# Kernel tuning notes

Hardware: AMD Instinct MI355X
Metric: run time of the kernel (lower is better)

The kernel has to match this reference:

```python
import jax, jax.numpy as jnp
import numpy as np

EPS = 1e-5
GROUPS = 32


def _groupnorm(x, gamma, beta):
    B, C, H, W = x.shape
    xr = x.reshape(B, GROUPS, C // GROUPS, H, W)
    mu = xr.mean(axis=(2, 3, 4), keepdims=True)
    var = xr.var(axis=(2, 3, 4), keepdims=True)
    xn = ((xr - mu) * jax.lax.rsqrt(var + EPS)).reshape(B, C, H, W)
    return xn * gamma[None, :, None, None] + beta[None, :, None, None]


def _conv1x1(x, w, b):
    # x: [B,C,H,W], w: [Cout,Cin], b: [Cout]
    return jnp.einsum('bchw,oc->bohw', x, w) + b[None, :, None, None]


def setup_inputs() -> dict:
    key = jax.random.key(0)
    ks = jax.random.split(key, 11)
    B, C, H, W = 4, 64, 64, 64
    s = 0.05  # weight scale for well-conditioned softmax
    inp = {
        'x': jax.random.normal(ks[0], (B, C, H, W), jnp.float32),
        'gn_gamma': jnp.ones((C,), jnp.float32),
        'gn_beta': jnp.zeros((C,), jnp.float32),
        'wq': jax.random.normal(ks[1], (C, C), jnp.float32) * s,
        'bq': jnp.zeros((C,), jnp.float32),
        'wk': jax.random.normal(ks[2], (C, C), jnp.float32) * s,
        'bk': jnp.zeros((C,), jnp.float32),
        'wv': jax.random.normal(ks[3], (C, C), jnp.float32) * s,
        'bv': jnp.zeros((C,), jnp.float32),
        'wp': jax.random.normal(ks[4], (C, C), jnp.float32) * s,
        'bp': jnp.zeros((C,), jnp.float32),
    }
    return inp


def reference(x, gn_gamma, gn_beta, wq, bq, wk, bk, wv, bv, wp, bp):
    B, C, H, W = x.shape
    h = _groupnorm(x, gn_gamma, gn_beta)
    q = _conv1x1(h, wq, bq)
    k = _conv1x1(h, wk, bk)
    v = _conv1x1(h, wv, bv)
    # scores over all spatial positions: [B,H,W,H,W]
    scale = 1.0 / jnp.sqrt(jnp.asarray(C, x.dtype))
    w = jnp.einsum('bchw,bcHW->bhwHW', q, k) * scale
    w = jax.nn.softmax(w.reshape(B, H, W, H * W), axis=-1).reshape(B, H, W, H, W)
    h = jnp.einsum('bhwHW,bcHW->bchw', w, v)
    h = _conv1x1(h, wp, bp)
    return x + h
```

## Files before the change

kernel.cpp:

```cpp
#include <hip/hip_runtime.h>
#include <stdint.h>

#define Bn 4
#define Cn 64
#define Sn 4096
#define Gn 32

typedef float v4f __attribute__((ext_vector_type(4)));
typedef short v8s __attribute__((ext_vector_type(8)));
typedef short v4s __attribute__((ext_vector_type(4)));

#define MFMA16(a,b,c) __builtin_amdgcn_mfma_f32_16x16x32_bf16((a),(b),(c),0,0,0)

#define QSC 0.18033688011112042f

__device__ __forceinline__ float bf2f(uint16_t u){
  union { uint32_t i; float f; } x; x.i = ((uint32_t)u) << 16; return x.f;
}
__device__ __forceinline__ uint16_t f2bf(float f){
  union { float f; uint32_t i; } x; x.f = f;
  uint32_t r = x.i + 0x7fffu + ((x.i >> 16) & 1u);
  return (uint16_t)(r >> 16);
}
__device__ __forceinline__ uint32_t cvtpk(float a, float b){
  uint32_t r;
  asm("v_cvt_pk_bf16_f32 %0, %1, %2" : "=v"(r) : "v"(a), "v"(b));
  return r;
}

__global__ __launch_bounds__(256) void gn_stats(
    const float* __restrict__ x,
    const float* __restrict__ wq, const float* __restrict__ wk,
    const float* __restrict__ wv, const float* __restrict__ wp,
    float* __restrict__ stats, uint16_t* __restrict__ Wbf)
{
  const int tid = threadIdx.x;
  if (blockIdx.x >= 128) {
    const int m = blockIdx.x - 128;
    const float* src = (m == 0) ? wq : (m == 1) ? wk : (m == 2) ? wv : wp;
    const float sc  = (m == 0) ? QSC : 1.f;
    uint16_t* dst = Wbf + (m << 12);
    #pragma unroll
    for (int i = 0; i < 4; ++i) {
      const int e = (tid << 4) + (i << 2);
      float4 v = *(const float4*)(src + e);
      v4s o;
      o[0] = (short)f2bf(v.x*sc); o[1] = (short)f2bf(v.y*sc);
      o[2] = (short)f2bf(v.z*sc); o[3] = (short)f2bf(v.w*sc);
      *(v4s*)(dst + e) = o;
    }
    return;
  }
  const float* base = x + (size_t)blockIdx.x * 8192;
  float sum = 0.f, sq = 0.f;
  #pragma unroll
  for (int i = 0; i < 8; ++i) {
    float4 v = *(const float4*)(base + ((i << 8) + tid)*4);
    sum += v.x + v.y + v.z + v.w;
    sq  += v.x*v.x + v.y*v.y + v.z*v.z + v.w*v.w;
  }
  #pragma unroll
  for (int off = 1; off < 64; off <<= 1) {
    sum += __shfl_xor(sum, off);
    sq  += __shfl_xor(sq, off);
  }
  __shared__ float red[8];
  const int w = tid >> 6;
  if ((tid & 63) == 0) { red[w] = sum; red[4+w] = sq; }
  __syncthreads();
  if (tid == 0) {
    float s = red[0]+red[1]+red[2]+red[3];
    float q = red[4]+red[5]+red[6]+red[7];
    float mean = s * (1.f/8192.f);
    float var  = q * (1.f/8192.f) - mean*mean;
    stats[blockIdx.x]       = mean;
    stats[128 + blockIdx.x] = rsqrtf(fmaxf(var, 0.f) + 1e-5f);
  }
}

__global__ __launch_bounds__(256) void gn_qkv(
    const float* __restrict__ xg, const float* __restrict__ gamma,
    const float* __restrict__ beta, const uint16_t* __restrict__ Wbf,
    const float* __restrict__ bq, const float* __restrict__ bk,
    const float* __restrict__ bv,
    const float* __restrict__ stats,
    uint16_t* __restrict__ Qg, uint16_t* __restrict__ Kg, uint16_t* __restrict__ Vg)
{
  __shared__ uint16_t Hs[16*72];
  const int tid  = threadIdx.x;
  const int w    = tid >> 6;
  const int lane = tid & 63;
  const int l15  = lane & 15;
  const int quad = lane >> 4;
  const int b      = blockIdx.x >> 8;
  const int s_base = (blockIdx.x & 255) << 4;

  {
    const int c = lane;
    const int g = c >> 1;
    const float mean = stats[b*Gn + g];
    const float rstd = stats[128 + b*Gn + g];
    const float ga = gamma[c], be = beta[c];
    float4 v = *(const float4*)(xg + ((size_t)b*Cn + c)*Sn + s_base + (w << 2));
    const int r0 = w << 2;
    Hs[(r0+0)*72 + c] = f2bf((v.x - mean)*rstd*ga + be);
    Hs[(r0+1)*72 + c] = f2bf((v.y - mean)*rstd*ga + be);
    Hs[(r0+2)*72 + c] = f2bf((v.z - mean)*rstd*ga + be);
    Hs[(r0+3)*72 + c] = f2bf((v.w - mean)*rstd*ga + be);
  }
  __syncthreads();

  v8s bh0 = *(const v8s*)(Hs + l15*72 + (quad << 3));
  v8s bh1 = *(const v8s*)(Hs + l15*72 + 32 + (quad << 3));

  #pragma unroll
  for (int t = 0; t < 3; ++t) {
    const int ot   = w*3 + t;
    const int wsel = ot >> 2;
    const int o16  = (ot & 3) << 4;
    const float* Bsel = (wsel == 0) ? bq : (wsel == 1) ? bk : bv;
    const float bsc   = (wsel == 0) ? QSC : 1.f;
    const uint16_t* Wr = Wbf + (wsel << 12) + (o16 + l15)*64 + (quad << 3);
    v8s a0 = *(const v8s*)(Wr);
    v8s a1 = *(const v8s*)(Wr + 32);
    v4f d = (v4f){0.f,0.f,0.f,0.f};
    d = MFMA16(a0, bh0, d);
    d = MFMA16(a1, bh1, d);
    const int s = s_base + l15;
    if (wsel <= 1) {
      v4s qv;
      #pragma unroll
      for (int r = 0; r < 4; ++r)
        qv[r] = (short)f2bf(d[r] + Bsel[o16 + (quad << 2) + r]*bsc);
      uint16_t* dst = (wsel == 0 ? Qg : Kg) + ((size_t)b*Sn + s)*64 + o16 + (quad << 2);
      *(v4s*)dst = qv;
    } else {
      #pragma unroll
      for (int r = 0; r < 4; ++r) {
        const int o = o16 + (quad << 2) + r;
        Vg[((size_t)b*Cn + o)*Sn + s] = f2bf(d[r] + Bsel[o]);
      }
    }
  }
}

__global__ __launch_bounds__(256, 4) void attn_split(
    const uint16_t* __restrict__ Qg, const uint16_t* __restrict__ Kg,
    const uint16_t* __restrict__ Vg,
    uint16_t* __restrict__ Opart, float* __restrict__ lpart)
{
  __shared__ uint16_t Ks[2][64*72];
  __shared__ uint16_t Vs[2][64*72];

  const int tid  = threadIdx.x;
  const int w    = tid >> 6;
  const int lane = tid & 63;
  const int l15  = lane & 15;
  const int quad = lane >> 4;
  const int bx    = blockIdx.x;
  const int split = bx & 7;
  const int qt    = (bx >> 3) & 31;
  const int b     = bx >> 8;
  const int i_base = qt << 7;
  const int j0     = split << 9;

  const uint16_t* Qb = Qg + ((size_t)b*Sn + i_base)*64;
  const uint16_t* Kb = Kg + (size_t)b*Sn*64;
  const uint16_t* Vb = Vg + (size_t)b*Cn*Sn;

  v8s qb[2][2];
  #pragma unroll
  for (int h = 0; h < 2; ++h) {
    const int row = (w << 5) + (h << 4) + l15;
    qb[h][0] = *(const v8s*)(Qb + row*64 + (quad << 3));
    qb[h][1] = *(const v8s*)(Qb + row*64 + 32 + (quad << 3));
  }

  const int e0 = tid << 3,         r0 = e0 >> 6, c0 = e0 & 63;
  const int e1 = (256 + tid) << 3, r1 = e1 >> 6, c1 = e1 & 63;

  *(v8s*)(Ks[0] + r0*72 + c0) = *(const v8s*)(Kb + j0*64 + e0);
  *(v8s*)(Ks[0] + r1*72 + c1) = *(const v8s*)(Kb + j0*64 + e1);
  *(v8s*)(Vs[0] + r0*72 + c0) = *(const v8s*)(Vb + (size_t)r0*Sn + j0 + c0);
  *(v8s*)(Vs[0] + r1*72 + c1) = *(const v8s*)(Vb + (size_t)r1*Sn + j0 + c1);

  const v8s ones8 = (v8s){0x3F80,0x3F80,0x3F80,0x3F80,0x3F80,0x3F80,0x3F80,0x3F80};

  v4f o_l[2];
  v4f o_acc[2][4];
  #pragma unroll
  for (int h = 0; h < 2; ++h) {
    o_l[h] = (v4f){0.f,0.f,0.f,0.f};
    #pragma unroll
    for (int nc = 0; nc < 4; ++nc) o_acc[h][nc] = (v4f){0.f,0.f,0.f,0.f};
  }

  __syncthreads();

  for (int kt = 0; kt < 8; ++kt) {
    const int cur = kt & 1;
    v8s kp0, kp1, vp0, vp1;
    if (kt < 7) {
      const int jb = j0 + ((kt + 1) << 6);
      kp0 = *(const v8s*)(Kb + jb*64 + e0);
      kp1 = *(const v8s*)(Kb + jb*64 + e1);
      vp0 = *(const v8s*)(Vb + (size_t)r0*Sn + jb + c0);
      vp1 = *(const v8s*)(Vb + (size_t)r1*Sn + jb + c1);
    }

    v8s ka[4][2];
    #pragma unroll
    for (int n = 0; n < 4; ++n) {
      const uint16_t* kr = Ks[cur] + ((n << 4) + l15)*72;
      ka[n][0] = *(const v8s*)(kr + (quad << 3));
      ka[n][1] = *(const v8s*)(kr + 32 + (quad << 3));
    }

    v8s pa[2][2];
    #pragma unroll
    for (int h = 0; h < 2; ++h) {
      v4f s[4];
      #pragma unroll
      for (int n = 0; n < 4; ++n) {
        v4f t = (v4f){0.f,0.f,0.f,0.f};
        t = MFMA16(ka[n][0], qb[h][0], t);
        t = MFMA16(ka[n][1], qb[h][1], t);
        s[n] = t;
      }
      union { v8s s8; uint32_t u[4]; } u0, u1;
      #pragma unroll
      for (int n = 0; n < 4; ++n) {
        const float p0 = __builtin_amdgcn_exp2f(s[n][0]);
        const float p1 = __builtin_amdgcn_exp2f(s[n][1]);
        const float p2 = __builtin_amdgcn_exp2f(s[n][2]);
        const float p3 = __builtin_amdgcn_exp2f(s[n][3]);
        const uint32_t w0 = cvtpk(p0, p1);
        const uint32_t w1 = cvtpk(p2, p3);
        if (n < 2) { u0.u[(n & 1)*2] = w0; u0.u[(n & 1)*2 + 1] = w1; }
        else       { u1.u[(n & 1)*2] = w0; u1.u[(n & 1)*2 + 1] = w1; }
      }
      pa[h][0] = u0.s8;
      pa[h][1] = u1.s8;
      o_l[h] = MFMA16(pa[h][0], ones8, o_l[h]);
      o_l[h] = MFMA16(pa[h][1], ones8, o_l[h]);
    }

    #pragma unroll
    for (int nc = 0; nc < 4; ++nc) {
      const uint16_t* vrow = Vs[cur] + ((nc << 4) + l15)*72;
      #pragma unroll
      for (int c = 0; c < 2; ++c) {
        union { v8s s8; v4s h4[2]; } vb;
        vb.h4[0] = *(const v4s*)(vrow + (c << 5) + (quad << 2));
        vb.h4[1] = *(const v4s*)(vrow + (c << 5) + 16 + (quad << 2));
        o_acc[0][nc] = MFMA16(pa[0][c], vb.s8, o_acc[0][nc]);
        o_acc[1][nc] = MFMA16(pa[1][c], vb.s8, o_acc[1][nc]);
      }
    }

    if (kt < 7) {
      const int nxt = cur ^ 1;
      *(v8s*)(Ks[nxt] + r0*72 + c0) = kp0;
      *(v8s*)(Ks[nxt] + r1*72 + c1) = kp1;
      *(v8s*)(Vs[nxt] + r0*72 + c0) = vp0;
      *(v8s*)(Vs[nxt] + r1*72 + c1) = vp1;
      __syncthreads();
    }
  }

  uint16_t* Ob = Opart + (size_t)bx*8192 + (size_t)(w << 5)*64;
  float*    lp = lpart + bx*128 + (w << 5);
  #pragma unroll
  for (int h = 0; h < 2; ++h)
    #pragma unroll
    for (int nc = 0; nc < 4; ++nc)
      #pragma unroll
      for (int r = 0; r < 4; ++r)
        Ob[((h << 4) + (quad << 2) + r)*64 + (nc << 4) + l15] = f2bf(o_acc[h][nc][r]);
  if (l15 == 0) {
    #pragma unroll
    for (int h = 0; h < 2; ++h)
      #pragma unroll
      for (int r = 0; r < 4; ++r)
        lp[(h << 4) + (quad << 2) + r] = o_l[h][r];
  }
}

__global__ __launch_bounds__(256) void proj_res(
    const uint16_t* __restrict__ Opart, const float* __restrict__ lpart,
    const uint16_t* __restrict__ Wbf, const float* __restrict__ bp,
    const float* __restrict__ xg, float* __restrict__ out)
{
  __shared__ uint16_t As[16*72];
  const int tid  = threadIdx.x;
  const int w    = tid >> 6;
  const int lane = tid & 63;
  const int l15  = lane & 15;
  const int quad = lane >> 4;
  const int b      = blockIdx.x >> 8;
  const int st     = blockIdx.x & 255;
  const int qt     = st >> 3;
  const int sub    = st & 7;
  const int s_base = st << 4;

  const uint16_t* po = Opart + (size_t)((b*32 + qt)*8)*8192 + (sub << 4)*64;
  const float*    pl = lpart + ((b*32 + qt)*8)*128 + (sub << 4);

  {
    const int e = tid << 2, row = tid >> 4, col = (tid & 15) << 2;
    float lsum = 0.f;
    #pragma unroll
    for (int sp = 0; sp < 8; ++sp) lsum += pl[sp*128 + row];
    const float linv = 1.f / lsum;
    float acc[4] = {0.f,0.f,0.f,0.f};
    #pragma unroll
    for (int sp = 0; sp < 8; ++sp) {
      v4s o = *(const v4s*)(po + (size_t)sp*8192 + e);
      #pragma unroll
      for (int j = 0; j < 4; ++j) acc[j] += bf2f((uint16_t)o[j]);
    }
    v4s a;
    #pragma unroll
    for (int j = 0; j < 4; ++j) a[j] = (short)f2bf(acc[j]*linv);
    *(v4s*)(As + row*72 + col) = a;
  }
  __syncthreads();

  v8s ba0 = *(const v8s*)(As + l15*72 + (quad << 3));
  v8s ba1 = *(const v8s*)(As + l15*72 + 32 + (quad << 3));

  const uint16_t* Wr = Wbf + (3 << 12) + ((w << 4) + l15)*64 + (quad << 3);
  v8s a0 = *(const v8s*)(Wr);
  v8s a1 = *(const v8s*)(Wr + 32);
  v4f d = (v4f){0.f,0.f,0.f,0.f};
  d = MFMA16(a0, ba0, d);
  d = MFMA16(a1, ba1, d);
  const int s = s_base + l15;
  #pragma unroll
  for (int r = 0; r < 4; ++r) {
    const int o = (w << 4) + (quad << 2) + r;
    const size_t idx = ((size_t)b*Cn + o)*Sn + s;
    out[idx] = d[r] + bp[o] + xg[idx];
  }
}

extern "C" void kernel_launch(void* const* d_in, const int* in_sizes, int n_in,
                              void* d_out, int out_size, void* d_ws, size_t ws_size,
                              hipStream_t stream)
{
  const float* x     = (const float*)d_in[0];
  const float* gamma = (const float*)d_in[1];
  const float* beta  = (const float*)d_in[2];
  const float* wq    = (const float*)d_in[3];
  const float* bq    = (const float*)d_in[4];
  const float* wk    = (const float*)d_in[5];
  const float* bk    = (const float*)d_in[6];
  const float* wv    = (const float*)d_in[7];
  const float* bv    = (const float*)d_in[8];
  const float* wp    = (const float*)d_in[9];
  const float* bp    = (const float*)d_in[10];

  float*    stats = (float*)d_ws;
  uint16_t* Wbf   = (uint16_t*)d_ws + 2048;
  uint16_t* Qg    = (uint16_t*)d_ws + 32768;
  uint16_t* Kg    = Qg + (size_t)Bn*Sn*Cn;
  uint16_t* Vg    = Kg + (size_t)Bn*Sn*Cn;
  uint16_t* Opart = Vg + (size_t)Bn*Sn*Cn;
  float*    lpart = (float*)(Opart + (size_t)1024*8192);
  float*    outp  = (float*)d_out;

  gn_stats  <<<132, 256, 0, stream>>>(x, wq, wk, wv, wp, stats, Wbf);
  gn_qkv    <<<1024, 256, 0, stream>>>(x, gamma, beta, Wbf, bq, bk, bv,
                                       stats, Qg, Kg, Vg);
  attn_split<<<1024, 256, 0, stream>>>(Qg, Kg, Vg, Opart, lpart);
  proj_res  <<<1024, 256, 0, stream>>>(Opart, lpart, Wbf, bp, x, outp);
}
```

Baseline: 113.6 us.

## Fuse split-KV reduction and output projection into attention via last-block counter

Removes the separate proj_res kernel. Each query tile keeps an atomic counter that gn_stats zeroes, and the last of the 8 split blocks to finish reduces the partial outputs, applies the Wp projection, bias and residual, and writes the final output. The K/V shared buffers are merged into one array so the tail can reuse LDS. s_setprio hints are also added around the MFMA sections. In exchange it drops a kernel launch and the gap between launches, but the tail work now runs serially in the last block of each tile.

```diff
diff --git a/kernel.cpp b/kernel.cpp
--- a/kernel.cpp
+++ b/kernel.cpp
@@ -32,11 +32,13 @@
     const float* __restrict__ x,
     const float* __restrict__ wq, const float* __restrict__ wk,
     const float* __restrict__ wv, const float* __restrict__ wp,
-    float* __restrict__ stats, uint16_t* __restrict__ Wbf)
+    float* __restrict__ stats, uint16_t* __restrict__ Wbf,
+    uint32_t* __restrict__ cnt)
 {
   const int tid = threadIdx.x;
   if (blockIdx.x >= 128) {
     const int m = blockIdx.x - 128;
+    if (tid < 32) cnt[(m << 5) + tid] = 0u;
     const float* src = (m == 0) ? wq : (m == 1) ? wk : (m == 2) ? wv : wp;
     const float sc  = (m == 0) ? QSC : 1.f;
     uint16_t* dst = Wbf + (m << 12);
@@ -147,10 +149,12 @@
 __global__ __launch_bounds__(256, 4) void attn_split(
     const uint16_t* __restrict__ Qg, const uint16_t* __restrict__ Kg,
     const uint16_t* __restrict__ Vg,
-    uint16_t* __restrict__ Opart, float* __restrict__ lpart)
+    uint16_t* __restrict__ Opart, float* __restrict__ lpart,
+    uint32_t* __restrict__ cnt, const uint16_t* __restrict__ Wbf,
+    const float* __restrict__ bp, const float* __restrict__ xg,
+    float* __restrict__ out)
 {
-  __shared__ uint16_t Ks[2][64*72];
-  __shared__ uint16_t Vs[2][64*72];
+  __shared__ uint16_t SM[18432];
 
   const int tid  = threadIdx.x;
   const int w    = tid >> 6;
@@ -179,10 +183,10 @@
   const int e0 = tid << 3,         r0 = e0 >> 6, c0 = e0 & 63;
   const int e1 = (256 + tid) << 3, r1 = e1 >> 6, c1 = e1 & 63;
 
-  *(v8s*)(Ks[0] + r0*72 + c0) = *(const v8s*)(Kb + j0*64 + e0);
-  *(v8s*)(Ks[0] + r1*72 + c1) = *(const v8s*)(Kb + j0*64 + e1);
-  *(v8s*)(Vs[0] + r0*72 + c0) = *(const v8s*)(Vb + (size_t)r0*Sn + j0 + c0);
-  *(v8s*)(Vs[0] + r1*72 + c1) = *(const v8s*)(Vb + (size_t)r1*Sn + j0 + c1);
+  *(v8s*)(SM + r0*72 + c0) = *(const v8s*)(Kb + j0*64 + e0);
+  *(v8s*)(SM + r1*72 + c1) = *(const v8s*)(Kb + j0*64 + e1);
+  *(v8s*)(SM + 9216 + r0*72 + c0) = *(const v8s*)(Vb + (size_t)r0*Sn + j0 + c0);
+  *(v8s*)(SM + 9216 + r1*72 + c1) = *(const v8s*)(Vb + (size_t)r1*Sn + j0 + c1);
 
   const v8s ones8 = (v8s){0x3F80,0x3F80,0x3F80,0x3F80,0x3F80,0x3F80,0x3F80,0x3F80};
 
@@ -198,7 +202,9 @@
   __syncthreads();
 
   for (int kt = 0; kt < 8; ++kt) {
-    const int cur = kt & 1;
+    const int co = (kt & 1)*4608;
+    uint16_t* const Kcur = SM + co;
+    uint16_t* const Vcur = SM + 9216 + co;
     v8s kp0, kp1, vp0, vp1;
     if (kt < 7) {
       const int jb = j0 + ((kt + 1) << 6);
@@ -211,7 +217,7 @@
     v8s ka[4][2];
     #pragma unroll
     for (int n = 0; n < 4; ++n) {
-      const uint16_t* kr = Ks[cur] + ((n << 4) + l15)*72;
+      const uint16_t* kr = Kcur + ((n << 4) + l15)*72;
       ka[n][0] = *(const v8s*)(kr + (quad << 3));
       ka[n][1] = *(const v8s*)(kr + 32 + (quad << 3));
     }
@@ -220,6 +226,7 @@
     #pragma unroll
     for (int h = 0; h < 2; ++h) {
       v4f s[4];
+      __builtin_amdgcn_s_setprio(1);
       #pragma unroll
       for (int n = 0; n < 4; ++n) {
         v4f t = (v4f){0.f,0.f,0.f,0.f};
@@ -227,6 +234,7 @@
         t = MFMA16(ka[n][1], qb[h][1], t);
         s[n] = t;
       }
+      __builtin_amdgcn_s_setprio(0);
       union { v8s s8; uint32_t u[4]; } u0, u1;
       #pragma unroll
       for (int n = 0; n < 4; ++n) {
@@ -245,9 +253,10 @@
       o_l[h] = MFMA16(pa[h][1], ones8, o_l[h]);
     }
 
+    __builtin_amdgcn_s_setprio(1);
     #pragma unroll
     for (int nc = 0; nc < 4; ++nc) {
-      const uint16_t* vrow = Vs[cur] + ((nc << 4) + l15)*72;
+      const uint16_t* vrow = Vcur + ((nc << 4) + l15)*72;
       #pragma unroll
       for (int c = 0; c < 2; ++c) {
         union { v8s s8; v4s h4[2]; } vb;
@@ -257,13 +266,14 @@
         o_acc[1][nc] = MFMA16(pa[1][c], vb.s8, o_acc[1][nc]);
       }
     }
+    __builtin_amdgcn_s_setprio(0);
 
     if (kt < 7) {
-      const int nxt = cur ^ 1;
-      *(v8s*)(Ks[nxt] + r0*72 + c0) = kp0;
-      *(v8s*)(Ks[nxt] + r1*72 + c1) = kp1;
-      *(v8s*)(Vs[nxt] + r0*72 + c0) = vp0;
-      *(v8s*)(Vs[nxt] + r1*72 + c1) = vp1;
+      const int no = ((kt & 1) ^ 1)*4608;
+      *(v8s*)(SM + no + r0*72 + c0) = kp0;
+      *(v8s*)(SM + no + r1*72 + c1) = kp1;
+      *(v8s*)(SM + 9216 + no + r0*72 + c0) = vp0;
+      *(v8s*)(SM + 9216 + no + r1*72 + c1) = vp1;
       __syncthreads();
     }
   }
@@ -284,63 +294,56 @@
       for (int r = 0; r < 4; ++r)
         lp[(h << 4) + (quad << 2) + r] = o_l[h][r];
   }
-}
-
-__global__ __launch_bounds__(256) void proj_res(
-    const uint16_t* __restrict__ Opart, const float* __restrict__ lpart,
-    const uint16_t* __restrict__ Wbf, const float* __restrict__ bp,
-    const float* __restrict__ xg, float* __restrict__ out)
-{
-  __shared__ uint16_t As[16*72];
-  const int tid  = threadIdx.x;
-  const int w    = tid >> 6;
-  const int lane = tid & 63;
-  const int l15  = lane & 15;
-  const int quad = lane >> 4;
-  const int b      = blockIdx.x >> 8;
-  const int st     = blockIdx.x & 255;
-  const int qt     = st >> 3;
-  const int sub    = st & 7;
-  const int s_base = st << 4;
-
-  const uint16_t* po = Opart + (size_t)((b*32 + qt)*8)*8192 + (sub << 4)*64;
-  const float*    pl = lpart + ((b*32 + qt)*8)*128 + (sub << 4);
-
-  {
-    const int e = tid << 2, row = tid >> 4, col = (tid & 15) << 2;
-    float lsum = 0.f;
-    #pragma unroll
-    for (int sp = 0; sp < 8; ++sp) lsum += pl[sp*128 + row];
-    const float linv = 1.f / lsum;
-    float acc[4] = {0.f,0.f,0.f,0.f};
-    #pragma unroll
-    for (int sp = 0; sp < 8; ++sp) {
-      v4s o = *(const v4s*)(po + (size_t)sp*8192 + e);
-      #pragma unroll
-      for (int j = 0; j < 4; ++j) acc[j] += bf2f((uint16_t)o[j]);
-    }
-    v4s a;
-    #pragma unroll
-    for (int j = 0; j < 4; ++j) a[j] = (short)f2bf(acc[j]*linv);
-    *(v4s*)(As + row*72 + col) = a;
-  }
-  __syncthreads();
-
-  v8s ba0 = *(const v8s*)(As + l15*72 + (quad << 3));
-  v8s ba1 = *(const v8s*)(As + l15*72 + 32 + (quad << 3));
-
-  const uint16_t* Wr = Wbf + (3 << 12) + ((w << 4) + l15)*64 + (quad << 3);
-  v8s a0 = *(const v8s*)(Wr);
-  v8s a1 = *(const v8s*)(Wr + 32);
-  v4f d = (v4f){0.f,0.f,0.f,0.f};
-  d = MFMA16(a0, ba0, d);
-  d = MFMA16(a1, ba1, d);
-  const int s = s_base + l15;
-  #pragma unroll
-  for (int r = 0; r < 4; ++r) {
-    const int o = (w << 4) + (quad << 2) + r;
-    const size_t idx = ((size_t)b*Cn + o)*Sn + s;
-    out[idx] = d[r] + bp[o] + xg[idx];
+
+  __threadfence();
+  __syncthreads();
+  __shared__ uint32_t sh_last;
+  const int bq = b*32 + qt;
+  if (tid == 0) sh_last = (atomicAdd(&cnt[bq], 1u) == 7u) ? 1u : 0u;
+  __syncthreads();
+  if (!sh_last) return;
+  __threadfence();
+
+  const uint16_t* poB = Opart + (size_t)bq*8*8192;
+  const float*    plB = lpart + (size_t)bq*8*128;
+  const uint16_t* Wr  = Wbf + (3 << 12) + ((w << 4) + l15)*64 + (quad << 3);
+  const v8s wa0 = *(const v8s*)(Wr);
+  const v8s wa1 = *(const v8s*)(Wr + 32);
+  const int mrow = tid >> 4, mcol = (tid & 15) << 2;
+
+  for (int sub = 0; sub < 8; ++sub) {
+    uint16_t* tA = SM + (sub & 1)*4608;
+    {
+      float lsum = 0.f;
+      #pragma unroll
+      for (int sp = 0; sp < 8; ++sp) lsum += plB[sp*128 + (sub << 4) + mrow];
+      const float linv = 1.f / lsum;
+      float acc[4] = {0.f,0.f,0.f,0.f};
+      const uint16_t* pp = poB + ((sub << 4) + mrow)*64 + mcol;
+      #pragma unroll
+      for (int sp = 0; sp < 8; ++sp) {
+        v4s o = *(const v4s*)(pp + (size_t)sp*8192);
+        #pragma unroll
+        for (int j = 0; j < 4; ++j) acc[j] += bf2f((uint16_t)o[j]);
+      }
+      v4s a;
+      #pragma unroll
+      for (int j = 0; j < 4; ++j) a[j] = (short)f2bf(acc[j]*linv);
+      *(v4s*)(tA + mrow*72 + mcol) = a;
+    }
+    __syncthreads();
+    v8s ba0 = *(const v8s*)(tA + l15*72 + (quad << 3));
+    v8s ba1 = *(const v8s*)(tA + l15*72 + 32 + (quad << 3));
+    v4f d = (v4f){0.f,0.f,0.f,0.f};
+    d = MFMA16(wa0, ba0, d);
+    d = MFMA16(wa1, ba1, d);
+    const int s = i_base + (sub << 4) + l15;
+    #pragma unroll
+    for (int r = 0; r < 4; ++r) {
+      const int o = (w << 4) + (quad << 2) + r;
+      const size_t idx = ((size_t)b*Cn + o)*Sn + s;
+      out[idx] = d[r] + bp[o] + xg[idx];
+    }
   }
 }
 
@@ -361,6 +364,7 @@
   const float* bp    = (const float*)d_in[10];
 
   float*    stats = (float*)d_ws;
+  uint32_t* cnt   = (uint32_t*)d_ws + 256;
   uint16_t* Wbf   = (uint16_t*)d_ws + 2048;
   uint16_t* Qg    = (uint16_t*)d_ws + 32768;
   uint16_t* Kg    = Qg + (size_t)Bn*Sn*Cn;
@@ -369,9 +373,9 @@
   float*    lpart = (float*)(Opart + (size_t)1024*8192);
   float*    outp  = (float*)d_out;
 
-  gn_stats  <<<132, 256, 0, stream>>>(x, wq, wk, wv, wp, stats, Wbf);
+  gn_stats  <<<132, 256, 0, stream>>>(x, wq, wk, wv, wp, stats, Wbf, cnt);
   gn_qkv    <<<1024, 256, 0, stream>>>(x, gamma, beta, Wbf, bq, bk, bv,
                                        stats, Qg, Kg, Vg);
-  attn_split<<<1024, 256, 0, stream>>>(Qg, Kg, Vg, Opart, lpart);
-  proj_res  <<<1024, 256, 0, stream>>>(Opart, lpart, Wbf, bp, x, outp);
-}
+  attn_split<<<1024, 256, 0, stream>>>(Qg, Kg, Vg, Opart, lpart, cnt,
+                                       Wbf, bp, x, outp);
+}
```

New measurement: 317.7 us. 180% more time.
